# Kernel optimization log

Measured on AMD Instinct MI355X. Metric: run time of the kernel, lower is better.

## Reference

```python
import jax, jax.numpy as jnp
import numpy as np

B = 4096
NUM_FEATURES = 2048
NUM_NEURONS = 1024
NUM_TARGETS = 8
NNZ1 = 65536
NNZ2 = 8192


def _sparse_linear(x, w, b, rows, cols, n_out):
    """y[b, o] = sum_{e: rows[e]==o} w[e] * x[b, cols[e]] + b[o].

    x: [B, n_in], w: [nnz], rows/cols: [nnz] int, b: [n_out].
    """
    prod = x[:, cols] * w  # [B, nnz] gather + elementwise
    # segment_sum reduces over leading axis -> work on [nnz, B]
    y = jax.ops.segment_sum(prod.T, rows, num_segments=n_out)  # [n_out, B]
    return y.T + b


def setup_inputs() -> dict:
    key = jax.random.key(0)
    ks = jax.random.split(key, 9)
    x = jax.random.normal(ks[0], (B, NUM_FEATURES), dtype=jnp.float32)
    w1 = jax.random.normal(ks[1], (NNZ1,), dtype=jnp.float32) * 0.05
    b1 = jax.random.normal(ks[2], (NUM_NEURONS,), dtype=jnp.float32) * 0.05
    w2 = jax.random.normal(ks[3], (NNZ2,), dtype=jnp.float32) * 0.05
    b2 = jax.random.normal(ks[4], (NUM_TARGETS,), dtype=jnp.float32) * 0.05
    conn1_out = jax.random.randint(ks[5], (NNZ1,), 0, NUM_NEURONS, dtype=jnp.int64 if jax.config.jax_enable_x64 else jnp.int32)
    conn1_in = jax.random.randint(ks[6], (NNZ1,), 0, NUM_FEATURES, dtype=conn1_out.dtype)
    conn2_out = jax.random.randint(ks[7], (NNZ2,), 0, NUM_TARGETS, dtype=conn1_out.dtype)
    conn2_in = jax.random.randint(ks[8], (NNZ2,), 0, NUM_NEURONS, dtype=conn1_out.dtype)
    return {
        "x": x, "w1": w1, "b1": b1, "w2": w2, "b2": b2,
        "conn1_out": conn1_out, "conn1_in": conn1_in,
        "conn2_out": conn2_out, "conn2_in": conn2_in,
    }


def reference(x, w1, b1, w2, b2, conn1_out, conn1_in, conn2_out, conn2_in):
    h = jax.nn.sigmoid(_sparse_linear(x, w1, b1, conn1_out, conn1_in, b1.shape[0]))
    out = _sparse_linear(h, w2, b2, conn2_out, conn2_in, b2.shape[0])
    # num_targets = 8 != 1, so no final sigmoid (matches CrossEntropyLoss path)
    return out
```

## Files before the change

### kernel.cpp

```cpp
#include <hip/hip_runtime.h>
#include <math.h>

#define BATCH 4096
#define NFEAT 2048
#define NNEUR 1024
#define NTGT  8
#define NNZ1  65536
#define NNZ2  8192

#define BM 128
#define BN 64
#define BK 64
#define KSTEPS (NFEAT / BK)

typedef short  bf16x8 __attribute__((ext_vector_type(8)));
typedef float  f32x4  __attribute__((ext_vector_type(4)));

#define OFF_W1F  ((size_t)0)
#define OFF_W2D  ((size_t)8388608)
#define OFF_W1P  ((size_t)8421376)

#define ZERO_FLOAT4 526336
#define OUT_FLOAT4  (BATCH * NTGT / 4)

__device__ __forceinline__ uint4 pk8(float4 lo, float4 hi) {
    uint4 r;
    asm("v_cvt_pk_bf16_f32 %0, %1, %2" : "=v"(r.x) : "v"(lo.x), "v"(lo.y));
    asm("v_cvt_pk_bf16_f32 %0, %1, %2" : "=v"(r.y) : "v"(lo.z), "v"(lo.w));
    asm("v_cvt_pk_bf16_f32 %0, %1, %2" : "=v"(r.z) : "v"(hi.x), "v"(hi.y));
    asm("v_cvt_pk_bf16_f32 %0, %1, %2" : "=v"(r.w) : "v"(hi.z), "v"(hi.w));
    return r;
}

__global__ void k_zero(float4* __restrict__ ws4, float4* __restrict__ out4,
                       const float* __restrict__ b2) {
    int i = blockIdx.x * blockDim.x + threadIdx.x;
    if (i < ZERO_FLOAT4) {
        ws4[i] = make_float4(0.f, 0.f, 0.f, 0.f);
    } else {
        int j = i - ZERO_FLOAT4;
        if (j < OUT_FLOAT4) {
            int p = (j & 1) * 4;
            out4[j] = make_float4(b2[p], b2[p + 1], b2[p + 2], b2[p + 3]);
        }
    }
}

__global__ void k_build(const float* __restrict__ w1, const int* __restrict__ c1o,
                        const int* __restrict__ c1i,
                        const float* __restrict__ w2, const int* __restrict__ c2o,
                        const int* __restrict__ c2i,
                        float* __restrict__ W1f, float* __restrict__ W2d) {
    int i = blockIdx.x * blockDim.x + threadIdx.x;
    if (i < NNZ1) {
        atomicAdd(&W1f[(size_t)c1o[i] * NFEAT + c1i[i]], w1[i]);
    } else {
        int j = i - NNZ1;
        if (j < NNZ2) atomicAdd(&W2d[c2i[j] * NTGT + c2o[j]], w2[j]);
    }
}

__global__ void k_pack(const float* __restrict__ W1f, unsigned short* __restrict__ W1p) {
    int u = blockIdx.x * blockDim.x + threadIdx.x;
    int lane  = u & 63;
    int kslot = (u >> 6) & 1;
    int i     = (u >> 7) & 3;
    int ks    = (u >> 9) & 31;
    int mt    = u >> 14;
    int row = mt * 64 + i * 16 + (lane & 15);
    int k   = ks * 64 + kslot * 32 + (lane >> 4) * 8;
    const float* src = &W1f[(size_t)row * NFEAT + k];
    float4 lo = *(const float4*)src;
    float4 hi = *(const float4*)(src + 4);
    ((uint4*)W1p)[u] = pk8(lo, hi);
}

__global__ __launch_bounds__(256) void k_gemm(const unsigned short* __restrict__ W1p,
                                              const float* __restrict__ x,
                                              const float* __restrict__ b1,
                                              const float* __restrict__ W2d,
                                              float* __restrict__ out) {
    __shared__ unsigned short ldsB[2][BN * BK];
    __shared__ float s_w2[BM][NTGT];
    __shared__ float s_b1[BM];
    __shared__ float s_pt[2][BN][NTGT];

    int bid = blockIdx.x;
    int xcd = bid & 7;
    int loc = bid >> 3;
    int m0  = ((xcd & 1) * 4 + (loc & 3)) * BM;
    int n0  = ((xcd >> 1) * 16 + (loc >> 2)) * BN;

    int tid  = threadIdx.x;
    int wv   = tid >> 6;
    int lane = tid & 63;
    int wm = wv >> 1, wn = wv & 1;
    int lr = lane & 15, lg = lane >> 4;

    for (int i = tid; i < BM * NTGT; i += 256)
        s_w2[i >> 3][i & 7] = W2d[(m0 + (i >> 3)) * NTGT + (i & 7)];
    if (tid < BM) s_b1[tid] = b1[m0 + tid];

    f32x4 zero4 = {0.f, 0.f, 0.f, 0.f};
    f32x4 acc[4][2];
#pragma unroll
    for (int i = 0; i < 4; ++i)
#pragma unroll
        for (int j = 0; j < 2; ++j) acc[i][j] = zero4;

    int mtA = (m0 >> 6) + wm;
    const bf16x8* gAf = (const bf16x8*)W1p + (size_t)mtA * 16384 + lane;

    int r0 = tid >> 3, s0 = tid & 7;
    const float* gB0 = &x[(size_t)(n0 + r0) * NFEAT + s0 * 8];
    const float* gB1 = gB0 + 32 * NFEAT;
    const int iw0 = r0 * 8 + (s0 ^ (r0 & 7));
    const int iw1 = iw0 + 256;

    bf16x8 Af0[8], Af1[8];
    float4 B0a, B0b, B0c, B0d;
    float4 B1a, B1b, B1c, B1d;
    bf16x8 bg0[2], bg1[2];

#define LOADSA0(T) do {                                             \
        _Pragma("unroll")                                           \
        for (int c = 0; c < 8; ++c) Af0[c] = gAf[(T) * 512 + c * 64]; } while (0)
#define LOADSA1(T) do {                                             \
        _Pragma("unroll")                                           \
        for (int c = 0; c < 8; ++c) Af1[c] = gAf[(T) * 512 + c * 64]; } while (0)
#define LOADSB0(T) do { int kk = (T) * BK;                          \
        B0a = *(const float4*)(gB0 + kk); B0b = *(const float4*)(gB0 + kk + 4); \
        B0c = *(const float4*)(gB1 + kk); B0d = *(const float4*)(gB1 + kk + 4); } while (0)
#define LOADSB1(T) do { int kk = (T) * BK;                          \
        B1a = *(const float4*)(gB0 + kk); B1b = *(const float4*)(gB0 + kk + 4); \
        B1c = *(const float4*)(gB1 + kk); B1d = *(const float4*)(gB1 + kk + 4); } while (0)

#define STORE0(BUF) do {                                            \
        uint4* dB = (uint4*)&ldsB[BUF][0];                          \
        dB[iw0] = pk8(B0a, B0b); dB[iw1] = pk8(B0c, B0d); } while (0)
#define STORE1(BUF) do {                                            \
        uint4* dB = (uint4*)&ldsB[BUF][0];                          \
        dB[iw0] = pk8(B1a, B1b); dB[iw1] = pk8(B1c, B1d); } while (0)

#define READF(BUF) do {                                             \
        const unsigned short* bB = ldsB[BUF];                       \
        _Pragma("unroll")                                           \
        for (int j = 0; j < 2; ++j) {                               \
            int rowb = wn * 32 + j * 16 + lr;                       \
            bg0[j] = *(const bf16x8*)&bB[(rowb * 8 + ((lg)     ^ (rowb & 7))) * 8]; \
            bg1[j] = *(const bf16x8*)&bB[(rowb * 8 + ((4 + lg) ^ (rowb & 7))) * 8]; \
        }                                                           \
    } while (0)

#define MFMAS0() do {                                               \
        _Pragma("unroll")                                           \
        for (int i = 0; i < 4; ++i)                                 \
            _Pragma("unroll")                                       \
            for (int j = 0; j < 2; ++j)                             \
                acc[i][j] = __builtin_amdgcn_mfma_f32_16x16x32_bf16(Af0[i * 2],     bg0[j], acc[i][j], 0, 0, 0); \
        _Pragma("unroll")                                           \
        for (int i = 0; i < 4; ++i)                                 \
            _Pragma("unroll")                                       \
            for (int j = 0; j < 2; ++j)                             \
                acc[i][j] = __builtin_amdgcn_mfma_f32_16x16x32_bf16(Af0[i * 2 + 1], bg1[j], acc[i][j], 0, 0, 0); \
    } while (0)
#define MFMAS1() do {                                               \
        _Pragma("unroll")                                           \
        for (int i = 0; i < 4; ++i)                                 \
            _Pragma("unroll")                                       \
            for (int j = 0; j < 2; ++j)                             \
                acc[i][j] = __builtin_amdgcn_mfma_f32_16x16x32_bf16(Af1[i * 2],     bg0[j], acc[i][j], 0, 0, 0); \
        _Pragma("unroll")                                           \
        for (int i = 0; i < 4; ++i)                                 \
            _Pragma("unroll")                                       \
            for (int j = 0; j < 2; ++j)                             \
                acc[i][j] = __builtin_amdgcn_mfma_f32_16x16x32_bf16(Af1[i * 2 + 1], bg1[j], acc[i][j], 0, 0, 0); \
    } while (0)

#define LDSFENCE() asm volatile("s_waitcnt lgkmcnt(0)" ::: "memory")

    LOADSB0(0);
    LOADSA0(0);
    LOADSB1(1);
    LOADSA1(1);
    STORE0(0);
    LDSFENCE();
    __builtin_amdgcn_s_barrier();

#pragma unroll 1
    for (int p = 0; p < 15; ++p) {
        int e = 2 * p;
        LOADSB0(e + 2);
        STORE1(1);
        READF(0);
        MFMAS0();
        LOADSA0(e + 2);
        LDSFENCE();
        __builtin_amdgcn_s_barrier();
        LOADSB1(e + 3);
        STORE0(0);
        READF(1);
        MFMAS1();
        LOADSA1(e + 3);
        LDSFENCE();
        __builtin_amdgcn_s_barrier();
    }
    STORE1(1);
    READF(0);
    MFMAS0();
    LDSFENCE();
    __builtin_amdgcn_s_barrier();
    READF(1);
    MFMAS1();

#undef LOADSA0
#undef LOADSA1
#undef LOADSB0
#undef LOADSB1
#undef STORE0
#undef STORE1
#undef READF
#undef MFMAS0
#undef MFMAS1
#undef LDSFENCE

    float pt[2][NTGT];
#pragma unroll
    for (int j = 0; j < 2; ++j)
#pragma unroll
        for (int t = 0; t < NTGT; ++t) pt[j][t] = 0.f;

#pragma unroll
    for (int i = 0; i < 4; ++i) {
#pragma unroll
        for (int r = 0; r < 4; ++r) {
            int ml = wm * 64 + i * 16 + lg * 4 + r;
            float bn = s_b1[ml];
#pragma unroll
            for (int j = 0; j < 2; ++j) {
                float h = 1.f / (1.f + __expf(-(acc[i][j][r] + bn)));
#pragma unroll
                for (int t = 0; t < NTGT; ++t)
                    pt[j][t] += h * s_w2[ml][t];
            }
        }
    }
#pragma unroll
    for (int j = 0; j < 2; ++j)
#pragma unroll
        for (int t = 0; t < NTGT; ++t) {
            float val = pt[j][t];
            val += __shfl_xor(val, 16, 64);
            val += __shfl_xor(val, 32, 64);
            pt[j][t] = val;
        }
    if (lg == 0) {
#pragma unroll
        for (int j = 0; j < 2; ++j) {
            int nl = wn * 32 + j * 16 + lr;
#pragma unroll
            for (int t = 0; t < NTGT; ++t)
                s_pt[wm][nl][t] = pt[j][t];
        }
    }
    __syncthreads();
    for (int idx = tid; idx < BN * NTGT; idx += 256) {
        int nl = idx >> 3, t = idx & 7;
        atomicAdd(&out[(size_t)(n0 + nl) * NTGT + t], s_pt[0][nl][t] + s_pt[1][nl][t]);
    }
}

extern "C" void kernel_launch(void* const* d_in, const int* in_sizes, int n_in,
                              void* d_out, int out_size, void* d_ws, size_t ws_size,
                              hipStream_t stream) {
    (void)in_sizes; (void)n_in; (void)out_size; (void)ws_size;
    const float* x   = (const float*)d_in[0];
    const float* w1  = (const float*)d_in[1];
    const float* b1  = (const float*)d_in[2];
    const float* w2  = (const float*)d_in[3];
    const float* b2  = (const float*)d_in[4];
    const int*   c1o = (const int*)d_in[5];
    const int*   c1i = (const int*)d_in[6];
    const int*   c2o = (const int*)d_in[7];
    const int*   c2i = (const int*)d_in[8];
    float* out = (float*)d_out;

    char* ws = (char*)d_ws;
    float*          W1f  = (float*)(ws + OFF_W1F);
    float*          W2d  = (float*)(ws + OFF_W2D);
    unsigned short* W1p  = (unsigned short*)(ws + OFF_W1P);

    k_zero<<<(ZERO_FLOAT4 + OUT_FLOAT4 + 255) / 256, 256, 0, stream>>>(
        (float4*)ws, (float4*)out, b2);

    k_build<<<(NNZ1 + NNZ2) / 256, 256, 0, stream>>>(w1, c1o, c1i, w2, c2o, c2i, W1f, W2d);

    k_pack<<<NNEUR * NFEAT / 8 / 256, 256, 0, stream>>>(W1f, W1p);

    k_gemm<<<(NNEUR / BM) * (BATCH / BN), 256, 0, stream>>>(W1p, x, b1, W2d, out);
}
```

Measured before the change: 52.59 us.

## Pre-pack x into MFMA fragment layout and drop LDS staging in GEMM

```diff
diff --git a/kernel.cpp b/kernel.cpp
--- a/kernel.cpp
+++ b/kernel.cpp
@@ -8,10 +8,7 @@
 #define NNZ1  65536
 #define NNZ2  8192
 
-#define BM 128
-#define BN 64
-#define BK 64
-#define KSTEPS (NFEAT / BK)
+#define KSTEPS (NFEAT / 32)
 
 typedef short  bf16x8 __attribute__((ext_vector_type(8)));
 typedef float  f32x4  __attribute__((ext_vector_type(4)));
@@ -19,6 +16,7 @@
 #define OFF_W1F  ((size_t)0)
 #define OFF_W2D  ((size_t)8388608)
 #define OFF_W1P  ((size_t)8421376)
+#define OFF_XP   ((size_t)12615680)
 
 #define ZERO_FLOAT4 526336
 #define OUT_FLOAT4  (BATCH * NTGT / 4)
@@ -62,171 +60,107 @@
 
 __global__ void k_pack(const float* __restrict__ W1f, unsigned short* __restrict__ W1p) {
     int u = blockIdx.x * blockDim.x + threadIdx.x;
-    int lane  = u & 63;
-    int kslot = (u >> 6) & 1;
-    int i     = (u >> 7) & 3;
-    int ks    = (u >> 9) & 31;
-    int mt    = u >> 14;
-    int row = mt * 64 + i * 16 + (lane & 15);
-    int k   = ks * 64 + kslot * 32 + (lane >> 4) * 8;
+    int lane = u & 63;
+    int i    = (u >> 6) & 3;
+    int T    = (u >> 8) & 63;
+    int mp   = u >> 14;
+    int row = mp * 64 + i * 16 + (lane & 15);
+    int k   = T * 32 + (lane >> 4) * 8;
     const float* src = &W1f[(size_t)row * NFEAT + k];
     float4 lo = *(const float4*)src;
     float4 hi = *(const float4*)(src + 4);
     ((uint4*)W1p)[u] = pk8(lo, hi);
 }
 
+__global__ void k_packx(const float* __restrict__ x, unsigned short* __restrict__ xp) {
+    int u = blockIdx.x * blockDim.x + threadIdx.x;
+    int lane = u & 63;
+    int j    = (u >> 6) & 3;
+    int T    = (u >> 8) & 63;
+    int nb   = u >> 14;
+    int row = nb * 64 + j * 16 + (lane & 15);
+    int k   = T * 32 + (lane >> 4) * 8;
+    const float* src = &x[(size_t)row * NFEAT + k];
+    float4 lo = *(const float4*)src;
+    float4 hi = *(const float4*)(src + 4);
+    ((uint4*)xp)[u] = pk8(lo, hi);
+}
+
 __global__ __launch_bounds__(256) void k_gemm(const unsigned short* __restrict__ W1p,
-                                              const float* __restrict__ x,
+                                              const unsigned short* __restrict__ xp,
                                               const float* __restrict__ b1,
                                               const float* __restrict__ W2d,
                                               float* __restrict__ out) {
-    __shared__ unsigned short ldsB[2][BN * BK];
-    __shared__ float s_w2[BM][NTGT];
-    __shared__ float s_b1[BM];
-    __shared__ float s_pt[2][BN][NTGT];
-
     int bid = blockIdx.x;
     int xcd = bid & 7;
-    int loc = bid >> 3;
-    int m0  = ((xcd & 1) * 4 + (loc & 3)) * BM;
-    int n0  = ((xcd >> 1) * 16 + (loc >> 2)) * BN;
+    int i5  = bid >> 3;
+    int nq  = xcd * 2 + (i5 & 1);
+    int mp  = i5 >> 1;
 
     int tid  = threadIdx.x;
     int wv   = tid >> 6;
     int lane = tid & 63;
-    int wm = wv >> 1, wn = wv & 1;
+    int nb   = nq * 4 + wv;
     int lr = lane & 15, lg = lane >> 4;
 
-    for (int i = tid; i < BM * NTGT; i += 256)
-        s_w2[i >> 3][i & 7] = W2d[(m0 + (i >> 3)) * NTGT + (i & 7)];
-    if (tid < BM) s_b1[tid] = b1[m0 + tid];
-
-    f32x4 zero4 = {0.f, 0.f, 0.f, 0.f};
-    f32x4 acc[4][2];
+    const bf16x8* gA = (const bf16x8*)W1p + (size_t)mp * 16384 + lane;
+    const bf16x8* gB = (const bf16x8*)xp  + (size_t)nb * 16384 + lane;
+
+    f32x4 acc[4][4];
 #pragma unroll
     for (int i = 0; i < 4; ++i)
 #pragma unroll
-        for (int j = 0; j < 2; ++j) acc[i][j] = zero4;
-
-    int mtA = (m0 >> 6) + wm;
-    const bf16x8* gAf = (const bf16x8*)W1p + (size_t)mtA * 16384 + lane;
-
-    int r0 = tid >> 3, s0 = tid & 7;
-    const float* gB0 = &x[(size_t)(n0 + r0) * NFEAT + s0 * 8];
-    const float* gB1 = gB0 + 32 * NFEAT;
-    const int iw0 = r0 * 8 + (s0 ^ (r0 & 7));
-    const int iw1 = iw0 + 256;
-
-    bf16x8 Af0[8], Af1[8];
-    float4 B0a, B0b, B0c, B0d;
-    float4 B1a, B1b, B1c, B1d;
-    bf16x8 bg0[2], bg1[2];
-
-#define LOADSA0(T) do {                                             \
-        _Pragma("unroll")                                           \
-        for (int c = 0; c < 8; ++c) Af0[c] = gAf[(T) * 512 + c * 64]; } while (0)
-#define LOADSA1(T) do {                                             \
-        _Pragma("unroll")                                           \
-        for (int c = 0; c < 8; ++c) Af1[c] = gAf[(T) * 512 + c * 64]; } while (0)
-#define LOADSB0(T) do { int kk = (T) * BK;                          \
-        B0a = *(const float4*)(gB0 + kk); B0b = *(const float4*)(gB0 + kk + 4); \
-        B0c = *(const float4*)(gB1 + kk); B0d = *(const float4*)(gB1 + kk + 4); } while (0)
-#define LOADSB1(T) do { int kk = (T) * BK;                          \
-        B1a = *(const float4*)(gB0 + kk); B1b = *(const float4*)(gB0 + kk + 4); \
-        B1c = *(const float4*)(gB1 + kk); B1d = *(const float4*)(gB1 + kk + 4); } while (0)
-
-#define STORE0(BUF) do {                                            \
-        uint4* dB = (uint4*)&ldsB[BUF][0];                          \
-        dB[iw0] = pk8(B0a, B0b); dB[iw1] = pk8(B0c, B0d); } while (0)
-#define STORE1(BUF) do {                                            \
-        uint4* dB = (uint4*)&ldsB[BUF][0];                          \
-        dB[iw0] = pk8(B1a, B1b); dB[iw1] = pk8(B1c, B1d); } while (0)
-
-#define READF(BUF) do {                                             \
-        const unsigned short* bB = ldsB[BUF];                       \
-        _Pragma("unroll")                                           \
-        for (int j = 0; j < 2; ++j) {                               \
-            int rowb = wn * 32 + j * 16 + lr;                       \
-            bg0[j] = *(const bf16x8*)&bB[(rowb * 8 + ((lg)     ^ (rowb & 7))) * 8]; \
-            bg1[j] = *(const bf16x8*)&bB[(rowb * 8 + ((4 + lg) ^ (rowb & 7))) * 8]; \
-        }                                                           \
-    } while (0)
-
+        for (int j = 0; j < 4; ++j) acc[i][j] = (f32x4){0.f, 0.f, 0.f, 0.f};
+
+    bf16x8 A0[4], B0[4], A1[4], B1[4];
+
+#define LOADS0(T) do {                                              \
+        _Pragma("unroll")                                           \
+        for (int c = 0; c < 4; ++c) {                               \
+            A0[c] = gA[(T) * 256 + c * 64];                         \
+            B0[c] = gB[(T) * 256 + c * 64];                         \
+        } } while (0)
+#define LOADS1(T) do {                                              \
+        _Pragma("unroll")                                           \
+        for (int c = 0; c < 4; ++c) {                               \
+            A1[c] = gA[(T) * 256 + c * 64];                         \
+            B1[c] = gB[(T) * 256 + c * 64];                         \
+        } } while (0)
 #define MFMAS0() do {                                               \
         _Pragma("unroll")                                           \
         for (int i = 0; i < 4; ++i)                                 \
             _Pragma("unroll")                                       \
-            for (int j = 0; j < 2; ++j)                             \
-                acc[i][j] = __builtin_amdgcn_mfma_f32_16x16x32_bf16(Af0[i * 2],     bg0[j], acc[i][j], 0, 0, 0); \
+            for (int j = 0; j < 4; ++j)                             \
+                acc[i][j] = __builtin_amdgcn_mfma_f32_16x16x32_bf16(A0[i], B0[j], acc[i][j], 0, 0, 0); \
+    } while (0)
+#define MFMAS1() do {                                               \
         _Pragma("unroll")                                           \
         for (int i = 0; i < 4; ++i)                                 \
             _Pragma("unroll")                                       \
-            for (int j = 0; j < 2; ++j)                             \
-                acc[i][j] = __builtin_amdgcn_mfma_f32_16x16x32_bf16(Af0[i * 2 + 1], bg1[j], acc[i][j], 0, 0, 0); \
+            for (int j = 0; j < 4; ++j)                             \
+                acc[i][j] = __builtin_amdgcn_mfma_f32_16x16x32_bf16(A1[i], B1[j], acc[i][j], 0, 0, 0); \
     } while (0)
-#define MFMAS1() do {                                               \
-        _Pragma("unroll")                                           \
-        for (int i = 0; i < 4; ++i)                                 \
-            _Pragma("unroll")                                       \
-            for (int j = 0; j < 2; ++j)                             \
-                acc[i][j] = __builtin_amdgcn_mfma_f32_16x16x32_bf16(Af1[i * 2],     bg0[j], acc[i][j], 0, 0, 0); \
-        _Pragma("unroll")                                           \
-        for (int i = 0; i < 4; ++i)                                 \
-            _Pragma("unroll")                                       \
-            for (int j = 0; j < 2; ++j)                             \
-                acc[i][j] = __builtin_amdgcn_mfma_f32_16x16x32_bf16(Af1[i * 2 + 1], bg1[j], acc[i][j], 0, 0, 0); \
-    } while (0)
-
-#define LDSFENCE() asm volatile("s_waitcnt lgkmcnt(0)" ::: "memory")
-
-    LOADSB0(0);
-    LOADSA0(0);
-    LOADSB1(1);
-    LOADSA1(1);
-    STORE0(0);
-    LDSFENCE();
-    __builtin_amdgcn_s_barrier();
-
+
+    LOADS0(0);
+    LOADS1(1);
 #pragma unroll 1
-    for (int p = 0; p < 15; ++p) {
-        int e = 2 * p;
-        LOADSB0(e + 2);
-        STORE1(1);
-        READF(0);
+    for (int p = 0; p < 31; ++p) {
         MFMAS0();
-        LOADSA0(e + 2);
-        LDSFENCE();
-        __builtin_amdgcn_s_barrier();
-        LOADSB1(e + 3);
-        STORE0(0);
-        READF(1);
+        LOADS0(2 * p + 2);
         MFMAS1();
-        LOADSA1(e + 3);
-        LDSFENCE();
-        __builtin_amdgcn_s_barrier();
-    }
-    STORE1(1);
-    READF(0);
+        LOADS1(2 * p + 3);
+    }
     MFMAS0();
-    LDSFENCE();
-    __builtin_amdgcn_s_barrier();
-    READF(1);
     MFMAS1();
 
-#undef LOADSA0
-#undef LOADSA1
-#undef LOADSB0
-#undef LOADSB1
-#undef STORE0
-#undef STORE1
-#undef READF
+#undef LOADS0
+#undef LOADS1
 #undef MFMAS0
 #undef MFMAS1
-#undef LDSFENCE
-
-    float pt[2][NTGT];
-#pragma unroll
-    for (int j = 0; j < 2; ++j)
+
+    float pt[4][NTGT];
+#pragma unroll
+    for (int j = 0; j < 4; ++j)
 #pragma unroll
         for (int t = 0; t < NTGT; ++t) pt[j][t] = 0.f;
 
@@ -234,19 +168,22 @@
     for (int i = 0; i < 4; ++i) {
 #pragma unroll
         for (int r = 0; r < 4; ++r) {
-            int ml = wm * 64 + i * 16 + lg * 4 + r;
-            float bn = s_b1[ml];
-#pragma unroll
-            for (int j = 0; j < 2; ++j) {
+            int m = mp * 64 + i * 16 + lg * 4 + r;
+            float bn = b1[m];
+            float4 w2lo = *(const float4*)&W2d[m * NTGT];
+            float4 w2hi = *(const float4*)&W2d[m * NTGT + 4];
+#pragma unroll
+            for (int j = 0; j < 4; ++j) {
                 float h = 1.f / (1.f + __expf(-(acc[i][j][r] + bn)));
-#pragma unroll
-                for (int t = 0; t < NTGT; ++t)
-                    pt[j][t] += h * s_w2[ml][t];
+                pt[j][0] += h * w2lo.x; pt[j][1] += h * w2lo.y;
+                pt[j][2] += h * w2lo.z; pt[j][3] += h * w2lo.w;
+                pt[j][4] += h * w2hi.x; pt[j][5] += h * w2hi.y;
+                pt[j][6] += h * w2hi.z; pt[j][7] += h * w2hi.w;
             }
         }
     }
 #pragma unroll
-    for (int j = 0; j < 2; ++j)
+    for (int j = 0; j < 4; ++j)
 #pragma unroll
         for (int t = 0; t < NTGT; ++t) {
             float val = pt[j][t];
@@ -256,17 +193,12 @@
         }
     if (lg == 0) {
 #pragma unroll
-        for (int j = 0; j < 2; ++j) {
-            int nl = wn * 32 + j * 16 + lr;
+        for (int j = 0; j < 4; ++j) {
+            int n = nb * 64 + j * 16 + lr;
 #pragma unroll
             for (int t = 0; t < NTGT; ++t)
-                s_pt[wm][nl][t] = pt[j][t];
-        }
-    }
-    __syncthreads();
-    for (int idx = tid; idx < BN * NTGT; idx += 256) {
-        int nl = idx >> 3, t = idx & 7;
-        atomicAdd(&out[(size_t)(n0 + nl) * NTGT + t], s_pt[0][nl][t] + s_pt[1][nl][t]);
+                atomicAdd(&out[(size_t)n * NTGT + t], pt[j][t]);
+        }
     }
 }
 
@@ -289,6 +221,7 @@
     float*          W1f  = (float*)(ws + OFF_W1F);
     float*          W2d  = (float*)(ws + OFF_W2D);
     unsigned short* W1p  = (unsigned short*)(ws + OFF_W1P);
+    unsigned short* xp   = (unsigned short*)(ws + OFF_XP);
 
     k_zero<<<(ZERO_FLOAT4 + OUT_FLOAT4 + 255) / 256, 256, 0, stream>>>(
         (float4*)ws, (float4*)out, b2);
@@ -296,6 +229,7 @@
     k_build<<<(NNZ1 + NNZ2) / 256, 256, 0, stream>>>(w1, c1o, c1i, w2, c2o, c2i, W1f, W2d);
 
     k_pack<<<NNEUR * NFEAT / 8 / 256, 256, 0, stream>>>(W1f, W1p);
-
-    k_gemm<<<(NNEUR / BM) * (BATCH / BN), 256, 0, stream>>>(W1p, x, b1, W2d, out);
-}
+    k_packx<<<BATCH * NFEAT / 8 / 256, 256, 0, stream>>>(x, xp);
+
+    k_gemm<<<256, 256, 0, stream>>>(W1p, xp, b1, W2d, out);
+}
```

New measurement: 69.90 us. 1.33x slower.
